# Optimization experiments

Hardware: AMD Instinct MI355X
Metric: run time of the kernel (lower is better)

## Reference

```python
import jax, jax.numpy as jnp
import numpy as np

N_NODES = 8192
IN_F = 256
OUT_F = 256
ALPHA = 0.2  # LeakyReLU negative slope


def setup_inputs() -> dict:
    key = jax.random.key(0)
    k1, k2, k3, k4 = jax.random.split(key, 4)
    X = jax.random.normal(k1, (N_NODES, IN_F), dtype=jnp.float32)
    A = jax.random.randint(k2, (N_NODES, N_NODES), 0, 2, dtype=jnp.int32)
    # torch nn.Linear weight layout: (out_features, in_features)
    W = jax.random.normal(k3, (OUT_F, IN_F), dtype=jnp.float32) * (1.0 / np.sqrt(IN_F))
    r = jax.random.normal(k4, (2 * OUT_F, 1), dtype=jnp.float32)
    return {"X": X, "A": A, "W": W, "r": r}


def reference(X, A, W, r):
    # Wh = X @ W^T  -> (N, F_out)
    Wh = X @ W.T
    # Split r so that cat([Wh_i, Wh_j]) @ r == Wh_i @ r_src + Wh_j @ r_dst
    F_out = Wh.shape[-1]
    r_src = r[:F_out, 0]   # (F,)
    r_dst = r[F_out:, 0]   # (F,)
    s_i = Wh @ r_src       # (N,)
    s_j = Wh @ r_dst       # (N,)
    e = s_i[:, None] + s_j[None, :]                      # (N, N)
    e = jnp.where(e >= 0, e, ALPHA * e)                  # LeakyReLU
    e = jnp.where(A == 0, -jnp.inf, e)                   # mask non-edges
    attention = jax.nn.softmax(e, axis=1)                # row-wise softmax
    output = attention @ Wh                              # (N, F_out)
    return jax.nn.gelu(output, approximate=False)        # torch F.gelu (exact)
```

## Files before the change

### kernel.cpp

```cpp
#include <hip/hip_runtime.h>
#include <hip/hip_bf16.h>

#define N_NODES 8192
#define NF      256
#define L2E     1.44269504088896341f

typedef __attribute__((ext_vector_type(8))) short short8;
typedef __attribute__((ext_vector_type(4))) short short4v;
typedef __attribute__((ext_vector_type(4))) float floatx4;

static __device__ __forceinline__ float bf2f(short s) {
    return __uint_as_float(((unsigned)(unsigned short)s) << 16);
}
static __device__ __forceinline__ short f2bf_rn(float f) {
    unsigned u = __float_as_uint(f) + 0x8000u;
    return (short)(u >> 16);
}
struct bfpair { short hi, lo; };
static __device__ __forceinline__ bfpair split_bf(float x) {
    bfpair p;
    p.hi = f2bf_rn(x);
    p.lo = f2bf_rn(x - bf2f(p.hi));
    return p;
}
static __device__ __forceinline__ void async16(const void* g, void* l) {
    __builtin_amdgcn_global_load_lds(
        (const __attribute__((address_space(1))) unsigned*)g,
        (__attribute__((address_space(3))) unsigned*)l, 16, 0, 0);
}

__global__ __launch_bounds__(256) void kx_split(const float* __restrict__ W,
                                                short* __restrict__ Whi,
                                                short* __restrict__ Wlo) {
    #pragma unroll
    for (int e = 0; e < 4; ++e) {
        const int i = blockIdx.x * 1024 + e * 256 + threadIdx.x;
        bfpair p = split_bf(W[i]);
        Whi[i] = p.hi;
        Wlo[i] = p.lo;
    }
}

__global__ __launch_bounds__(512) void k1_gemm(const float* __restrict__ X,
                                               const short* __restrict__ Whi,
                                               const short* __restrict__ Wlo,
                                               const float* __restrict__ r,
                                               short* __restrict__ WhT,
                                               float* __restrict__ sp_src,
                                               float* __restrict__ sp_dst) {
    __shared__ float Xs[32 * 256];

    const int tid = threadIdx.x;
    const int w = tid >> 6, lane = tid & 63;
    const int q = lane >> 4, m = lane & 15;
    const int rh = w >> 2, cq = w & 3;
    const int i_base = blockIdx.x * 32;

    #pragma unroll
    for (int v = 0; v < 4; ++v) {
        const int rowv = w * 4 + v;
        const int c = lane ^ (rowv & 7);
        async16(X + (size_t)(i_base + rowv) * NF + c * 4, &Xs[rowv * 256]);
    }
    __syncthreads();

    floatx4 acc[4] = {};
    const int xrow = rh * 16 + m;
    const int r7 = xrow & 7;
    #pragma unroll
    for (int ks = 0; ks < 8; ++ks) {
        const int c0 = ks * 8 + q * 2;
        float4 f0 = *(const float4*)(&Xs[xrow * 256 + ((c0 ^ r7) * 4)]);
        float4 f1 = *(const float4*)(&Xs[xrow * 256 + (((c0 + 1) ^ r7) * 4)]);
        const float xsv[8] = {f0.x, f0.y, f0.z, f0.w, f1.x, f1.y, f1.z, f1.w};
        short8 xh, xl;
        #pragma unroll
        for (int c = 0; c < 8; ++c) {
            bfpair p = split_bf(xsv[c]);
            xh[c] = p.hi; xl[c] = p.lo;
        }
        #pragma unroll
        for (int nt = 0; nt < 4; ++nt) {
            const int n = cq * 64 + nt * 16 + m;
            short8 wh = *(const short8*)(Whi + n * NF + ks * 32 + q * 8);
            short8 wl = *(const short8*)(Wlo + n * NF + ks * 32 + q * 8);
            acc[nt] = __builtin_amdgcn_mfma_f32_16x16x32_bf16(xh, wh, acc[nt], 0, 0, 0);
            acc[nt] = __builtin_amdgcn_mfma_f32_16x16x32_bf16(xl, wh, acc[nt], 0, 0, 0);
            acc[nt] = __builtin_amdgcn_mfma_f32_16x16x32_bf16(xh, wl, acc[nt], 0, 0, 0);
        }
    }

    const int i0 = i_base + rh * 16 + q * 4;
    float vs[4] = {0.f, 0.f, 0.f, 0.f}, vd[4] = {0.f, 0.f, 0.f, 0.f};
    #pragma unroll
    for (int nt = 0; nt < 4; ++nt) {
        const int n = cq * 64 + nt * 16 + m;
        short4v v;
        #pragma unroll
        for (int r2 = 0; r2 < 4; ++r2) v[r2] = f2bf_rn(acc[nt][r2]);
        *(short4v*)(WhT + (size_t)n * N_NODES + i0) = v;
        const float rs = r[n], rd = r[NF + n];
        #pragma unroll
        for (int r2 = 0; r2 < 4; ++r2) {
            vs[r2] = fmaf(acc[nt][r2], rs, vs[r2]);
            vd[r2] = fmaf(acc[nt][r2], rd, vd[r2]);
        }
    }
    #pragma unroll
    for (int mask = 1; mask <= 8; mask <<= 1) {
        #pragma unroll
        for (int r2 = 0; r2 < 4; ++r2) {
            vs[r2] += __shfl_xor(vs[r2], mask);
            vd[r2] += __shfl_xor(vd[r2], mask);
        }
    }
    if (m == 0) {
        #pragma unroll
        for (int r2 = 0; r2 < 4; ++r2) {
            sp_src[cq * N_NODES + i0 + r2] = vs[r2];
            sp_dst[cq * N_NODES + i0 + r2] = vd[r2];
        }
    }
}

__global__ __launch_bounds__(256) void k2_sv(const float* __restrict__ sp_src,
                                             const float* __restrict__ sp_dst,
                                             float* __restrict__ s_src,
                                             float* __restrict__ s_dst,
                                             float* __restrict__ pmax) {
    __shared__ float red[256];
    const int tid = threadIdx.x;
    const int i = blockIdx.x * 256 + tid;
    float ss = 0.f, sd = 0.f;
    #pragma unroll
    for (int nb = 0; nb < 4; ++nb) {
        ss += sp_src[nb * N_NODES + i];
        sd += sp_dst[nb * N_NODES + i];
    }
    s_src[i] = ss;
    s_dst[i] = sd;
    red[tid] = sd;
    __syncthreads();
    for (int off = 128; off > 0; off >>= 1) {
        if (tid < off) red[tid] = fmaxf(red[tid], red[tid + off]);
        __syncthreads();
    }
    if (tid == 0) pmax[blockIdx.x] = red[0];
}

static __device__ __forceinline__ void pgroup(const int4 a, const floatx4 t,
                                              const float s_i, const float d_i,
                                              float* p) {
    const int av[4] = {a.x, a.y, a.z, a.w};
    #pragma unroll
    for (int c = 0; c < 4; ++c) {
        float sum = s_i + t[c];
        float lr  = fmaxf(sum, 0.2f * sum);
        float pp  = __builtin_amdgcn_exp2f(fmaf(lr, L2E, d_i));
        p[c] = (av[c] != 0) ? pp : 0.0f;
    }
}

__global__ __launch_bounds__(1024) void k4_attn(const int* __restrict__ Adj,
                                                const short* __restrict__ WhT,
                                                const float* __restrict__ s_dst,
                                                const float* __restrict__ s_src,
                                                const float* __restrict__ pmax,
                                                float* __restrict__ out) {
    __shared__ union {
        short B[4 * 256 * 64];
        float red[16 * 8 * 4 * 64];
    } sm;
    __shared__ float denred[128];

    const int tid = threadIdx.x;
    const int w = tid >> 6, lane = tid & 63;
    const int q = lane >> 4, m = lane & 15;
    const int rh = w >> 3, ch = (w >> 2) & 1, jq = w & 3;
    const int i0 = blockIdx.x * 32;
    const int row = i0 + rh * 16 + m;

    float M = pmax[0];
    #pragma unroll
    for (int b = 1; b < 32; ++b) M = fmaxf(M, pmax[b]);
    const float s_i = s_src[row];
    const float e0 = s_i + M;
    const float d_i = -fmaxf(e0, 0.2f * e0) * L2E;

    const int ug = w >> 2;
    const int jqs = w & 3;
    const int srow = lane >> 3;
    const int schunk = (lane & 7) ^ srow;
    const short* gB = WhT + (size_t)(ug * 64 + srow) * N_NODES + jqs * 64 + schunk * 8;
    short* ldsB = sm.B + (jqs * 256 + ug * 64) * 64;

    const int* Arow = Adj + (size_t)row * N_NODES + jq * 64 + q * 8;
    const float* tb = s_dst + jq * 64 + q * 8;

    floatx4 acc[8] = {{0.f,0.f,0.f,0.f}};
    #pragma unroll
    for (int nt = 0; nt < 8; ++nt) acc[nt] = (floatx4){0.f,0.f,0.f,0.f};
    float den = 0.f;

    #pragma unroll
    for (int v = 0; v < 8; ++v)
        async16(gB + v * 8 * N_NODES, ldsB + v * 8 * 64);
    int4 a0 = *(const int4*)(Arow);
    int4 a1 = *(const int4*)(Arow + 4);
    int4 a2 = *(const int4*)(Arow + 32);
    int4 a3 = *(const int4*)(Arow + 36);
    __syncthreads();

    for (int s = 0; s < 32; ++s) {
        const int offn = (s < 31) ? (s + 1) * 256 : s * 256;
        int4 na0 = *(const int4*)(Arow + offn);
        int4 na1 = *(const int4*)(Arow + offn + 4);
        int4 na2 = *(const int4*)(Arow + offn + 32);
        int4 na3 = *(const int4*)(Arow + offn + 36);
        const int ts = s * 256;
        floatx4 t0 = *(const floatx4*)(tb + ts);
        floatx4 t1 = *(const floatx4*)(tb + ts + 4);
        floatx4 t2 = *(const floatx4*)(tb + ts + 32);
        floatx4 t3 = *(const floatx4*)(tb + ts + 36);

        float p[16];
        pgroup(a0, t0, s_i, d_i, p);
        pgroup(a1, t1, s_i, d_i, p + 4);
        pgroup(a2, t2, s_i, d_i, p + 8);
        pgroup(a3, t3, s_i, d_i, p + 12);

        short8 af0, af1;
        #pragma unroll
        for (int c = 0; c < 8; ++c) { af0[c] = f2bf_rn(p[c]); af1[c] = f2bf_rn(p[8 + c]); }
        float ds = 0.f;
        #pragma unroll
        for (int c = 0; c < 16; ++c) ds += p[c];
        den += ds;

        const short* Bj = sm.B + jq * 256 * 64;
        #pragma unroll
        for (int nt = 0; nt < 8; ++nt) {
            const int n = ch * 128 + nt * 16 + m;
            const short* bp = Bj + n * 64;
            const int sw = n & 7;
            short8 b0 = *(const short8*)(bp + ((q ^ sw) * 8));
            short8 b1 = *(const short8*)(bp + (((q + 4) ^ sw) * 8));
            acc[nt] = __builtin_amdgcn_mfma_f32_16x16x32_bf16(af0, b0, acc[nt], 0, 0, 0);
            acc[nt] = __builtin_amdgcn_mfma_f32_16x16x32_bf16(af1, b1, acc[nt], 0, 0, 0);
        }
        a0 = na0; a1 = na1; a2 = na2; a3 = na3;

        __syncthreads();
        if (s < 31) {
            const int go = (s + 1) * 256;
            #pragma unroll
            for (int v = 0; v < 8; ++v)
                async16(gB + go + v * 8 * N_NODES, ldsB + v * 8 * 64);
            __syncthreads();
        }
    }

    den += __shfl_xor(den, 16);
    den += __shfl_xor(den, 32);
    if (ch == 0 && lane < 16) denred[rh * 64 + jq * 16 + lane] = den;
    #pragma unroll
    for (int nt = 0; nt < 8; ++nt)
        #pragma unroll
        for (int rg = 0; rg < 4; ++rg)
            sm.red[((w * 8 + nt) * 4 + rg) * 64 + lane] = acc[nt][rg];
    __syncthreads();

    float invd[4];
    #pragma unroll
    for (int rg = 0; rg < 4; ++rg) {
        const int rr = rh * 64 + q * 4 + rg;
        invd[rg] = 1.0f / fmaxf(denred[rr] + denred[rr + 16] +
                                denred[rr + 32] + denred[rr + 48], 1e-30f);
    }
    const int wb = rh * 8 + ch * 4;
    #pragma unroll
    for (int t2 = 0; t2 < 2; ++t2) {
        const int nt = jq * 2 + t2;
        #pragma unroll
        for (int rg = 0; rg < 4; ++rg) {
            float v = sm.red[(((wb + 0) * 8 + nt) * 4 + rg) * 64 + lane]
                    + sm.red[(((wb + 1) * 8 + nt) * 4 + rg) * 64 + lane]
                    + sm.red[(((wb + 2) * 8 + nt) * 4 + rg) * 64 + lane]
                    + sm.red[(((wb + 3) * 8 + nt) * 4 + rg) * 64 + lane];
            float x = v * invd[rg];
            float g = 0.5f * x * (1.0f + erff(x * 0.70710678118f));
            out[(size_t)(i0 + rh * 16 + q * 4 + rg) * NF + ch * 128 + nt * 16 + m] = g;
        }
    }
}

extern "C" void kernel_launch(void* const* d_in, const int* in_sizes, int n_in,
                              void* d_out, int out_size, void* d_ws, size_t ws_size,
                              hipStream_t stream) {
    const float* X = (const float*)d_in[0];
    const int*   A = (const int*)d_in[1];
    const float* W = (const float*)d_in[2];
    const float* r = (const float*)d_in[3];
    float* out = (float*)d_out;

    char* wsp = (char*)d_ws;
    short* WhT    = (short*)wsp;                    wsp += (size_t)NF * N_NODES * 2;
    short* Whi    = (short*)wsp;                    wsp += NF * NF * 2;
    short* Wlo    = (short*)wsp;                    wsp += NF * NF * 2;
    float* sp_src = (float*)wsp;                    wsp += 4 * N_NODES * 4;
    float* sp_dst = (float*)wsp;                    wsp += 4 * N_NODES * 4;
    float* s_src  = (float*)wsp;                    wsp += N_NODES * 4;
    float* s_dst  = (float*)wsp;                    wsp += N_NODES * 4;
    float* pmax   = (float*)wsp;

    kx_split<<<64, 256, 0, stream>>>(W, Whi, Wlo);
    k1_gemm<<<256, 512, 0, stream>>>(X, Whi, Wlo, r, WhT, sp_src, sp_dst);
    k2_sv<<<32, 256, 0, stream>>>(sp_src, sp_dst, s_src, s_dst, pmax);
    k4_attn<<<256, 1024, 0, stream>>>(A, WhT, s_dst, s_src, pmax, out);
}
```

Measured before the change: 481.4 us.

## Double-buffer WhT tiles in LDS and halve the column step per iteration

The attention kernel now keeps two 128-column WhT tiles in LDS and prefetches the next tile asynchronously while MFMAs run on the current one. This replaces the single-buffer scheme, which needed two barriers per step and left the loads exposed. The column step per iteration drops from 256 to 128, so each wave does one MFMA per n-tile instead of two, and the adjacency and s_dst values are prefetched one step ahead. The loop runs twice as many iterations, so barrier count and per-iteration overhead rise, and it depends on async16 completing before the single barrier at the end of each step.

```diff
diff --git a/kernel.cpp b/kernel.cpp
--- a/kernel.cpp
+++ b/kernel.cpp
@@ -168,7 +168,7 @@
                                                 const float* __restrict__ pmax,
                                                 float* __restrict__ out) {
     __shared__ union {
-        short B[4 * 256 * 64];
+        short B[2][256][128];
         float red[16 * 8 * 4 * 64];
     } sm;
     __shared__ float denred[128];
@@ -187,77 +187,69 @@
     const float e0 = s_i + M;
     const float d_i = -fmaxf(e0, 0.2f * e0) * L2E;
 
-    const int ug = w >> 2;
-    const int jqs = w & 3;
-    const int srow = lane >> 3;
-    const int schunk = (lane & 7) ^ srow;
-    const short* gB = WhT + (size_t)(ug * 64 + srow) * N_NODES + jqs * 64 + schunk * 8;
-    short* ldsB = sm.B + (jqs * 256 + ug * 64) * 64;
-
-    const int* Arow = Adj + (size_t)row * N_NODES + jq * 64 + q * 8;
-    const float* tb = s_dst + jq * 64 + q * 8;
-
-    floatx4 acc[8] = {{0.f,0.f,0.f,0.f}};
-    #pragma unroll
-    for (int nt = 0; nt < 8; ++nt) acc[nt] = (floatx4){0.f,0.f,0.f,0.f};
+    const int nloc = lane >> 4;
+    const int scl = lane & 15;
+    const short* gB[4];
+    #pragma unroll
+    for (int v = 0; v < 4; ++v) {
+        const int n = w * 16 + v * 4 + nloc;
+        const int c = scl ^ (n & 7);
+        gB[v] = WhT + (size_t)n * N_NODES + c * 8;
+    }
+
+    const int* Ap = Adj + (size_t)row * N_NODES + jq * 32 + q * 8;
+    const float* tp = s_dst + jq * 32 + q * 8;
+
+    floatx4 acc[8];
+    #pragma unroll
+    for (int nt = 0; nt < 8; ++nt) acc[nt] = (floatx4){0.f, 0.f, 0.f, 0.f};
     float den = 0.f;
 
     #pragma unroll
-    for (int v = 0; v < 8; ++v)
-        async16(gB + v * 8 * N_NODES, ldsB + v * 8 * 64);
-    int4 a0 = *(const int4*)(Arow);
-    int4 a1 = *(const int4*)(Arow + 4);
-    int4 a2 = *(const int4*)(Arow + 32);
-    int4 a3 = *(const int4*)(Arow + 36);
+    for (int v = 0; v < 4; ++v)
+        async16(gB[v], &sm.B[0][w * 16 + v * 4][0]);
+    int4 a0 = *(const int4*)(Ap);
+    int4 a1 = *(const int4*)(Ap + 4);
+    floatx4 t0 = *(const floatx4*)(tp);
+    floatx4 t1 = *(const floatx4*)(tp + 4);
     __syncthreads();
 
-    for (int s = 0; s < 32; ++s) {
-        const int offn = (s < 31) ? (s + 1) * 256 : s * 256;
-        int4 na0 = *(const int4*)(Arow + offn);
-        int4 na1 = *(const int4*)(Arow + offn + 4);
-        int4 na2 = *(const int4*)(Arow + offn + 32);
-        int4 na3 = *(const int4*)(Arow + offn + 36);
-        const int ts = s * 256;
-        floatx4 t0 = *(const floatx4*)(tb + ts);
-        floatx4 t1 = *(const floatx4*)(tb + ts + 4);
-        floatx4 t2 = *(const floatx4*)(tb + ts + 32);
-        floatx4 t3 = *(const floatx4*)(tb + ts + 36);
-
-        float p[16];
+    for (int s = 0; s < 64; ++s) {
+        const int cur = s & 1;
+
+        if (s < 63) {
+            const int go = (s + 1) * 128;
+            #pragma unroll
+            for (int v = 0; v < 4; ++v)
+                async16(gB[v] + go, &sm.B[cur ^ 1][w * 16 + v * 4][0]);
+        }
+        const int offn = ((s < 63) ? (s + 1) : s) * 128;
+        int4 na0 = *(const int4*)(Ap + offn);
+        int4 na1 = *(const int4*)(Ap + offn + 4);
+        floatx4 nt0 = *(const floatx4*)(tp + offn);
+        floatx4 nt1 = *(const floatx4*)(tp + offn + 4);
+
+        float p[8];
         pgroup(a0, t0, s_i, d_i, p);
         pgroup(a1, t1, s_i, d_i, p + 4);
-        pgroup(a2, t2, s_i, d_i, p + 8);
-        pgroup(a3, t3, s_i, d_i, p + 12);
-
-        short8 af0, af1;
-        #pragma unroll
-        for (int c = 0; c < 8; ++c) { af0[c] = f2bf_rn(p[c]); af1[c] = f2bf_rn(p[8 + c]); }
-        float ds = 0.f;
-        #pragma unroll
-        for (int c = 0; c < 16; ++c) ds += p[c];
-        den += ds;
-
-        const short* Bj = sm.B + jq * 256 * 64;
+
+        short8 af;
+        #pragma unroll
+        for (int c = 0; c < 8; ++c) af[c] = f2bf_rn(p[c]);
+        #pragma unroll
+        for (int c = 0; c < 8; ++c) den += p[c];
+
+        const short* Bb = &sm.B[cur][0][0];
         #pragma unroll
         for (int nt = 0; nt < 8; ++nt) {
             const int n = ch * 128 + nt * 16 + m;
-            const short* bp = Bj + n * 64;
-            const int sw = n & 7;
-            short8 b0 = *(const short8*)(bp + ((q ^ sw) * 8));
-            short8 b1 = *(const short8*)(bp + (((q + 4) ^ sw) * 8));
-            acc[nt] = __builtin_amdgcn_mfma_f32_16x16x32_bf16(af0, b0, acc[nt], 0, 0, 0);
-            acc[nt] = __builtin_amdgcn_mfma_f32_16x16x32_bf16(af1, b1, acc[nt], 0, 0, 0);
-        }
-        a0 = na0; a1 = na1; a2 = na2; a3 = na3;
-
+            const int sc = (jq * 4 + q) ^ (n & 7);
+            short8 b0 = *(const short8*)(Bb + n * 128 + sc * 8);
+            acc[nt] = __builtin_amdgcn_mfma_f32_16x16x32_bf16(af, b0, acc[nt], 0, 0, 0);
+        }
+
+        a0 = na0; a1 = na1; t0 = nt0; t1 = nt1;
         __syncthreads();
-        if (s < 31) {
-            const int go = (s + 1) * 256;
-            #pragma unroll
-            for (int v = 0; v < 8; ++v)
-                async16(gB + go + v * 8 * N_NODES, ldsB + v * 8 * 64);
-            __syncthreads();
-        }
     }
 
     den += __shfl_xor(den, 16);
```

New measurement: 481.1 us. Within noise of the previous version (-0.1%).
